# Optimization experiments

Hardware: AMD Instinct MI355X
Metric: run time of the kernel (lower is better)

Reference implementation:

```python
import jax, jax.numpy as jnp
import numpy as np

B, C, W, H = 32, 128, 128, 128  # batch, channels, window_size, prediction_horizon
KAPPA = 10.0

def setup_inputs() -> dict:
    key = jax.random.key(0)
    k1, k2, k3, k4 = jax.random.split(key, 4)
    x_t = jax.random.normal(k1, (B, C, W), dtype=jnp.float32)
    # d are observation timestamps in [0, H), compared against ref_t = linspace(0, H, H)
    d = jax.random.uniform(k2, (B, C, W), dtype=jnp.float32) * H
    # m is an observation mask/weight in (0, 1]; avoid exact zeros for log(m)
    m = jax.random.uniform(k3, (B, C, W), dtype=jnp.float32, minval=1e-3, maxval=1.0)
    kernel = jax.random.normal(k4, (W,), dtype=jnp.float32) * 0.1
    return {"x_t": x_t, "d": d, "m": m, "kernel": kernel}

def reference(x_t, d, m, kernel):
    # ref_t: [H], matches torch.linspace(0, H, H)
    ref_t = jnp.linspace(0.0, H, H, dtype=x_t.dtype)
    # norm: [B,C,W,H] squared time differences
    norm = (d[..., None] - ref_t) ** 2
    alpha = jnp.log1p(jnp.exp(kernel))[None, None, :, None]  # softplus, [1,1,W,1]
    logm = jnp.log(m)[..., None]                             # [B,C,W,1]
    # low-intensity interpolation (softmax over window dim W)
    s = -alpha * norm + logm                                 # [B,C,W,H]
    w = jax.nn.logsumexp(s, axis=2)                          # [B,C,H]
    w1 = jnp.exp(s - w[:, :, None, :])                       # softmax weights
    y = jnp.einsum('bcwh,bcw->bch', w1, x_t)
    # high-intensity (transient) interpolation with sharper kernel kappa*alpha
    s_t = -KAPPA * alpha * norm + logm
    wt_lse = jax.nn.logsumexp(s_t, axis=2)
    w_t = jnp.exp(s_t - wt_lse[:, :, None, :])
    y_trans = jnp.einsum('bcwh,bcw->bch', w_t, x_t)
    return (y, w, y_trans)
```

## Files before the change

### kernel.cpp

```cpp
#include <hip/hip_runtime.h>
#include <hip/hip_bf16.h>

#define NB 32
#define NC 128
#define NW 128
#define NH 128
#define BCH (NB * NC * NH)

__global__ __launch_bounds__(64) void sci_kernel(
    const void* __restrict__ xp, const void* __restrict__ dp,
    const void* __restrict__ mp, const void* __restrict__ kp,
    void* __restrict__ outp)
{
    const int bc  = blockIdx.x;
    const int tid = threadIdx.x;
    const int ll  = tid & 31;
    const int wbase = (tid >> 5) * 64;

    __shared__ float4 tile[NW];

    const unsigned short* du16 = (const unsigned short*)dp;
    bool is_bf16 = true;
    #pragma unroll
    for (int i = 0; i < 64; i += 2) {
        float v = __uint_as_float(((unsigned int)du16[i]) << 16);
        is_bf16 = is_bf16 && (v >= 0.0f) && (v <= 129.0f);
    }

    const float LOG2E = 1.4426950408889634f;
    #pragma unroll
    for (int j = 0; j < 2; ++j) {
        const int w = tid + 64 * j;
        const int base = bc * NW + w;
        float dv, mv, xv, kv;
        if (is_bf16) {
            dv = __bfloat162float(((const __hip_bfloat16*)dp)[base]);
            mv = __bfloat162float(((const __hip_bfloat16*)mp)[base]);
            xv = __bfloat162float(((const __hip_bfloat16*)xp)[base]);
            kv = __bfloat162float(((const __hip_bfloat16*)kp)[w]);
        } else {
            dv = ((const float*)dp)[base];
            mv = ((const float*)mp)[base];
            xv = ((const float*)xp)[base];
            kv = ((const float*)kp)[w];
        }
        float A2  = log1pf(__expf(kv)) * LOG2E;
        float sA2 = sqrtf(A2);
        tile[w] = make_float4(sA2, sA2 * dv, mv, mv * xv);
    }
    __syncthreads();

    float rh[4];
    #pragma unroll
    for (int j = 0; j < 4; ++j) rh[j] = (float)(ll + 32 * j) * (128.0f / 127.0f);

    float mna[4] = {3.0e38f, 3.0e38f, 3.0e38f, 3.0e38f};
    #pragma unroll 8
    for (int i = 0; i < 64; ++i) {
        float2 q = *(const float2*)&tile[wbase + i];
        #pragma unroll
        for (int j = 0; j < 4; ++j) {
            float t = __builtin_fmaf(-q.x, rh[j], q.y);
            mna[j] = fminf(mna[j], fabsf(t));
        }
    }
    float mn[4];
    #pragma unroll
    for (int j = 0; j < 4; ++j) {
        float o = __shfl_xor(mna[j], 32);
        float a = fminf(mna[j], o);
        mn[j] = a * a;
    }

    float s1[4] = {0.f, 0.f, 0.f, 0.f}, a1[4] = {0.f, 0.f, 0.f, 0.f};
    float s2[4] = {0.f, 0.f, 0.f, 0.f}, a2[4] = {0.f, 0.f, 0.f, 0.f};
    #pragma unroll 2
    for (int i = 0; i < 64; ++i) {
        float4 q = tile[wbase + i];
        #pragma unroll
        for (int j = 0; j < 4; ++j) {
            float t  = __builtin_fmaf(-q.x, rh[j], q.y);
            float v  = __builtin_fmaf(-t, t, mn[j]);
            float g1 = __builtin_amdgcn_exp2f(v);
            float sq = g1 * g1;
            float p4 = sq * sq;
            float p8 = p4 * p4;
            float g2 = p8 * sq;
            s1[j] = __builtin_fmaf(q.z, g1, s1[j]);
            a1[j] = __builtin_fmaf(q.w, g1, a1[j]);
            s2[j] = __builtin_fmaf(q.z, g2, s2[j]);
            a2[j] = __builtin_fmaf(q.w, g2, a2[j]);
        }
    }

    #pragma unroll
    for (int j = 0; j < 4; ++j) {
        s1[j] += __shfl_xor(s1[j], 32);
        a1[j] += __shfl_xor(a1[j], 32);
        s2[j] += __shfl_xor(s2[j], 32);
        a2[j] += __shfl_xor(a2[j], 32);
    }

    if (tid < 32) {
        const float LN2 = 0.6931471805599453f;
        const int obase = bc * NH + ll;
        #pragma unroll
        for (int j = 0; j < 4; ++j) {
            float y  = a1[j] * __builtin_amdgcn_rcpf(s1[j]);
            float wv = (__builtin_amdgcn_logf(s1[j]) - mn[j]) * LN2;
            float yt = a2[j] * __builtin_amdgcn_rcpf(s2[j]);
            const int o = obase + 32 * j;
            if (is_bf16) {
                __hip_bfloat16* o16 = (__hip_bfloat16*)outp;
                o16[o]           = __float2bfloat16(y);
                o16[BCH + o]     = __float2bfloat16(wv);
                o16[2 * BCH + o] = __float2bfloat16(yt);
            } else {
                float* o32 = (float*)outp;
                o32[o]           = y;
                o32[BCH + o]     = wv;
                o32[2 * BCH + o] = yt;
            }
        }
    }
}

extern "C" void kernel_launch(void* const* d_in, const int* in_sizes, int n_in,
                              void* d_out, int out_size, void* d_ws, size_t ws_size,
                              hipStream_t stream) {
    const void* x_t = d_in[0];
    const void* d   = d_in[1];
    const void* m   = d_in[2];
    const void* k   = d_in[3];
    dim3 grid(NB * NC);
    dim3 block(64);
    hipLaunchKernelGGL(sci_kernel, grid, block, 0, stream, x_t, d, m, k, d_out);
}
```

Baseline: 83.10 us.

## Split window reduction across two wavefronts per block with shared-memory combine

Blocks now run 128 threads (two wavefronts) instead of 64. Each wavefront reduces half of the window dimension for all 128 horizon points, and the partial minima and sums are combined through shared memory with extra barriers. This halves the serial loop length per thread and doubles the number of wavefronts in flight per block. The cost is extra shared-memory traffic and two additional __syncthreads, and the final write is spread over all 128 threads.

```diff
diff --git a/kernel.cpp b/kernel.cpp
--- a/kernel.cpp
+++ b/kernel.cpp
@@ -7,17 +7,20 @@
 #define NH 128
 #define BCH (NB * NC * NH)
 
-__global__ __launch_bounds__(64) void sci_kernel(
+__global__ __launch_bounds__(128, 8) void sci_kernel(
     const void* __restrict__ xp, const void* __restrict__ dp,
     const void* __restrict__ mp, const void* __restrict__ kp,
     void* __restrict__ outp)
 {
-    const int bc  = blockIdx.x;
-    const int tid = threadIdx.x;
-    const int ll  = tid & 31;
-    const int wbase = (tid >> 5) * 64;
+    const int bc   = blockIdx.x;
+    const int tid  = threadIdx.x;
+    const int wv   = tid >> 6;
+    const int ll   = tid & 31;
+    const int wbase = (wv << 6) + ((tid >> 5) & 1) * 32;
 
     __shared__ float4 tile[NW];
+    __shared__ float  mnbuf[2][NH];
+    __shared__ float4 pbuf[2][NH];
 
     const unsigned short* du16 = (const unsigned short*)dp;
     bool is_bf16 = true;
@@ -28,25 +31,23 @@
     }
 
     const float LOG2E = 1.4426950408889634f;
-    #pragma unroll
-    for (int j = 0; j < 2; ++j) {
-        const int w = tid + 64 * j;
-        const int base = bc * NW + w;
+    {
+        const int base = bc * NW + tid;
         float dv, mv, xv, kv;
         if (is_bf16) {
             dv = __bfloat162float(((const __hip_bfloat16*)dp)[base]);
             mv = __bfloat162float(((const __hip_bfloat16*)mp)[base]);
             xv = __bfloat162float(((const __hip_bfloat16*)xp)[base]);
-            kv = __bfloat162float(((const __hip_bfloat16*)kp)[w]);
+            kv = __bfloat162float(((const __hip_bfloat16*)kp)[tid]);
         } else {
             dv = ((const float*)dp)[base];
             mv = ((const float*)mp)[base];
             xv = ((const float*)xp)[base];
-            kv = ((const float*)kp)[w];
+            kv = ((const float*)kp)[tid];
         }
         float A2  = log1pf(__expf(kv)) * LOG2E;
         float sA2 = sqrtf(A2);
-        tile[w] = make_float4(sA2, sA2 * dv, mv, mv * xv);
+        tile[tid] = make_float4(sA2, sA2 * dv, mv, mv * xv);
     }
     __syncthreads();
 
@@ -56,7 +57,7 @@
 
     float mna[4] = {3.0e38f, 3.0e38f, 3.0e38f, 3.0e38f};
     #pragma unroll 8
-    for (int i = 0; i < 64; ++i) {
+    for (int i = 0; i < 32; ++i) {
         float2 q = *(const float2*)&tile[wbase + i];
         #pragma unroll
         for (int j = 0; j < 4; ++j) {
@@ -64,18 +65,24 @@
             mna[j] = fminf(mna[j], fabsf(t));
         }
     }
+    #pragma unroll
+    for (int j = 0; j < 4; ++j) mna[j] = fminf(mna[j], __shfl_xor(mna[j], 32));
+    if ((tid & 63) < 32) {
+        #pragma unroll
+        for (int j = 0; j < 4; ++j) mnbuf[wv][ll + 32 * j] = mna[j];
+    }
+    __syncthreads();
     float mn[4];
     #pragma unroll
     for (int j = 0; j < 4; ++j) {
-        float o = __shfl_xor(mna[j], 32);
-        float a = fminf(mna[j], o);
+        float a = fminf(mnbuf[0][ll + 32 * j], mnbuf[1][ll + 32 * j]);
         mn[j] = a * a;
     }
 
     float s1[4] = {0.f, 0.f, 0.f, 0.f}, a1[4] = {0.f, 0.f, 0.f, 0.f};
     float s2[4] = {0.f, 0.f, 0.f, 0.f}, a2[4] = {0.f, 0.f, 0.f, 0.f};
-    #pragma unroll 2
-    for (int i = 0; i < 64; ++i) {
+    #pragma unroll 4
+    for (int i = 0; i < 32; ++i) {
         float4 q = tile[wbase + i];
         #pragma unroll
         for (int j = 0; j < 4; ++j) {
@@ -100,27 +107,37 @@
         s2[j] += __shfl_xor(s2[j], 32);
         a2[j] += __shfl_xor(a2[j], 32);
     }
+    if ((tid & 63) < 32) {
+        #pragma unroll
+        for (int j = 0; j < 4; ++j)
+            pbuf[wv][ll + 32 * j] = make_float4(s1[j], a1[j], s2[j], a2[j]);
+    }
+    __syncthreads();
 
-    if (tid < 32) {
+    {
+        float4 P0 = pbuf[0][tid];
+        float4 P1 = pbuf[1][tid];
+        float S1 = P0.x + P1.x, A1 = P0.y + P1.y;
+        float S2 = P0.z + P1.z, A2 = P0.w + P1.w;
+        float a  = fminf(mnbuf[0][tid], mnbuf[1][tid]);
+        float mnh = a * a;
+
         const float LN2 = 0.6931471805599453f;
-        const int obase = bc * NH + ll;
-        #pragma unroll
-        for (int j = 0; j < 4; ++j) {
-            float y  = a1[j] * __builtin_amdgcn_rcpf(s1[j]);
-            float wv = (__builtin_amdgcn_logf(s1[j]) - mn[j]) * LN2;
-            float yt = a2[j] * __builtin_amdgcn_rcpf(s2[j]);
-            const int o = obase + 32 * j;
-            if (is_bf16) {
-                __hip_bfloat16* o16 = (__hip_bfloat16*)outp;
-                o16[o]           = __float2bfloat16(y);
-                o16[BCH + o]     = __float2bfloat16(wv);
-                o16[2 * BCH + o] = __float2bfloat16(yt);
-            } else {
-                float* o32 = (float*)outp;
-                o32[o]           = y;
-                o32[BCH + o]     = wv;
-                o32[2 * BCH + o] = yt;
-            }
+        float y  = A1 * __builtin_amdgcn_rcpf(S1);
+        float wvo = (__builtin_amdgcn_logf(S1) - mnh) * LN2;
+        float yt = A2 * __builtin_amdgcn_rcpf(S2);
+
+        const int o = bc * NH + tid;
+        if (is_bf16) {
+            __hip_bfloat16* o16 = (__hip_bfloat16*)outp;
+            o16[o]           = __float2bfloat16(y);
+            o16[BCH + o]     = __float2bfloat16(wvo);
+            o16[2 * BCH + o] = __float2bfloat16(yt);
+        } else {
+            float* o32 = (float*)outp;
+            o32[o]           = y;
+            o32[BCH + o]     = wvo;
+            o32[2 * BCH + o] = yt;
         }
     }
 }
@@ -133,6 +150,6 @@
     const void* m   = d_in[2];
     const void* k   = d_in[3];
     dim3 grid(NB * NC);
-    dim3 block(64);
+    dim3 block(128);
     hipLaunchKernelGGL(sci_kernel, grid, block, 0, stream, x_t, d, m, k, d_out);
 }
```

Result: no change. 83.93 us (+1.0%).
